# Performance work log

Measured on AMD Instinct MI355X. Metric: run time of the kernel, lower is better.

## Reference

```python
import jax, jax.numpy as jnp
import numpy as np

N = 100000      # nodes
E = 1600000     # edges (avg degree 16)
D_IN, HID, D_OUT = 128, 64, 64


def setup_inputs() -> dict:
    key = jax.random.key(0)
    ks = jax.random.split(key, 32)
    rn = lambda k, shape, s=0.1: jax.random.normal(k, shape, jnp.float32) * s
    inp = {
        "x": jax.random.normal(ks[0], (N, D_IN), jnp.float32),
        "edge_index": jax.random.randint(ks[1], (2, E), 0, N, dtype=jnp.int32),
        # GAT layer 1: in=128, heads=2, C=64, concat -> 128
        "w1": rn(ks[2], (D_IN, 2 * HID)), "as1": rn(ks[3], (2, HID)),
        "ad1": rn(ks[4], (2, HID)), "b1": rn(ks[5], (2 * HID,)),
        # GAT layer 2: in=128, heads=2, C=64, concat -> 128
        "w2": rn(ks[6], (2 * HID, 2 * HID)), "as2": rn(ks[7], (2, HID)),
        "ad2": rn(ks[8], (2, HID)), "b2": rn(ks[9], (2 * HID,)),
        # GAT layer 3: in=128, heads=1, C=64, mean -> 64
        "w3": rn(ks[10], (2 * HID, D_OUT)), "as3": rn(ks[11], (1, D_OUT)),
        "ad3": rn(ks[12], (1, D_OUT)), "b3": rn(ks[13], (D_OUT,)),
        # BatchNorm (eval mode: running stats)
        "g1": 1.0 + rn(ks[14], (2 * HID,)), "be1": rn(ks[15], (2 * HID,)),
        "m1": rn(ks[16], (2 * HID,), 0.01), "v1": 1.0 + 0.1 * jax.random.uniform(ks[17], (2 * HID,)),
        "g2": 1.0 + rn(ks[18], (2 * HID,)), "be2": rn(ks[19], (2 * HID,)),
        "m2": rn(ks[20], (2 * HID,), 0.01), "v2": 1.0 + 0.1 * jax.random.uniform(ks[21], (2 * HID,)),
        "g3": 1.0 + rn(ks[22], (D_OUT,)), "be3": rn(ks[23], (D_OUT,)),
        "m3": rn(ks[24], (D_OUT,), 0.01), "v3": 1.0 + 0.1 * jax.random.uniform(ks[25], (D_OUT,)),
    }
    return inp


def _gat(h, W, a_s, a_d, b, src, dst, n, heads, concat):
    """PyG GATConv (eval, add_self_loops already applied to src/dst)."""
    C = a_s.shape[1]
    xl = (h @ W).reshape(n, heads, C)                      # [N,H,C]
    es = jnp.sum(xl * a_s, axis=-1)                        # [N,H] att_src . x
    ed = jnp.sum(xl * a_d, axis=-1)                        # [N,H]
    e = jax.nn.leaky_relu(es[src] + ed[dst], 0.2)          # [E',H]
    mx = jax.ops.segment_max(e, dst, num_segments=n)       # segment softmax over dst
    ex = jnp.exp(e - mx[dst])
    den = jax.ops.segment_sum(ex, dst, num_segments=n)
    alpha = ex / (den[dst] + 1e-16)                        # [E',H]
    out = jax.ops.segment_sum(xl[src] * alpha[:, :, None], dst, num_segments=n)
    out = out.reshape(n, heads * C) if concat else out.mean(axis=1)
    return out + b


def _bn(z, g, be, m, v):
    return (z - m) * jax.lax.rsqrt(v + 1e-5) * g + be


def reference(x, edge_index, w1, as1, ad1, b1, w2, as2, ad2, b2, w3, as3, ad3, b3,
              g1, be1, m1, v1, g2, be2, m2, v2, g3, be3, m3, v3):
    n = x.shape[0]
    loop = jnp.arange(n, dtype=edge_index.dtype)
    src = jnp.concatenate([edge_index[0], loop])           # GATConv add_self_loops=True
    dst = jnp.concatenate([edge_index[1], loop])
    z = jax.nn.relu(_bn(_gat(x, w1, as1, ad1, b1, src, dst, n, 2, True), g1, be1, m1, v1))
    z = jax.nn.relu(_bn(_gat(z, w2, as2, ad2, b2, src, dst, n, 2, True), g2, be2, m2, v2))
    z = _bn(_gat(z, w3, as3, ad3, b3, src, dst, n, 1, False), g3, be3, m3, v3)
    return z
```

## Files before the change

kernel.cpp:

```cpp
#include <hip/hip_runtime.h>
#include <hip/hip_bf16.h>
#include <cstdint>
#include <cstddef>

#define SCAN_CHUNK 2048
#define NBLK 512
#define BSH 8

typedef short bf16x8 __attribute__((ext_vector_type(8)));
typedef float f32x4 __attribute__((ext_vector_type(4)));

__device__ __forceinline__ float leaky02(float x) { return x > 0.f ? x : 0.2f * x; }
__device__ __forceinline__ float bflo(unsigned u) { return __uint_as_float(u << 16); }
__device__ __forceinline__ float bfhi(unsigned u) { return __uint_as_float(u & 0xFFFF0000u); }
__device__ __forceinline__ unsigned short f2bf(float f) {
  __hip_bfloat16 h = __float2bfloat16(f);
  return *(unsigned short*)&h;
}
__device__ __forceinline__ unsigned pack2bf(float a, float b) {
  return (unsigned)f2bf(a) | ((unsigned)f2bf(b) << 16);
}

__global__ void scan_pass1(const int* __restrict__ cnt, int* __restrict__ bsum, int n) {
  __shared__ int red[4];
  int b = blockIdx.x, t = threadIdx.x;
  int base = b * SCAN_CHUNK;
  int s = 0;
  for (int i = t; i < SCAN_CHUNK; i += 256) {
    int idx = base + i;
    if (idx < n) s += cnt[idx];
  }
  for (int off = 32; off; off >>= 1) s += __shfl_xor(s, off);
  int lane = t & 63, wid = t >> 6;
  if (lane == 0) red[wid] = s;
  __syncthreads();
  if (t == 0) bsum[b] = red[0] + red[1] + red[2] + red[3];
}

__global__ void scan_pass2(int* __restrict__ bsum, int nb, int* __restrict__ totp) {
  if (threadIdx.x == 0) {
    int run = 0;
    for (int i = 0; i < nb; ++i) { int v = bsum[i]; bsum[i] = run; run += v; }
    *totp = run;
  }
}

__global__ void scan_pass3(const int* __restrict__ cnt, const int* __restrict__ bsum,
                           int* __restrict__ out, int n) {
  __shared__ int wsum[4];
  int b = blockIdx.x, t = threadIdx.x;
  int idx0 = b * SCAN_CHUNK + t * 8;
  int vals[8];
  int s = 0;
#pragma unroll
  for (int i = 0; i < 8; ++i) {
    int id = idx0 + i;
    int v = (id < n) ? cnt[id] : 0;
    vals[i] = s; s += v;
  }
  int lane = t & 63, wid = t >> 6;
  int incl = s;
  for (int off = 1; off < 64; off <<= 1) {
    int o = __shfl_up(incl, off);
    if (lane >= off) incl += o;
  }
  if (lane == 63) wsum[wid] = incl;
  __syncthreads();
  if (t == 0) { int r = 0; for (int i = 0; i < 4; ++i) { int v = wsum[i]; wsum[i] = r; r += v; } }
  __syncthreads();
  int texcl = incl - s + wsum[wid] + bsum[b];
#pragma unroll
  for (int i = 0; i < 8; ++i) {
    int id = idx0 + i;
    if (id < n) out[id] = texcl + vals[i];
  }
}

__global__ void bucketA(const int* __restrict__ dst, int* __restrict__ H,
                        int E, int N, int NB, int echunk, int nchunk) {
  __shared__ int hist[512];
  int b = blockIdx.x, t = threadIdx.x;
  hist[t] = 0; hist[t + 256] = 0;
  __syncthreads();
  int e0 = b * echunk, e1 = min(E, e0 + echunk);
  for (int e = e0 + t; e < e1; e += 256) atomicAdd(&hist[dst[e] >> BSH], 1);
  int n0 = b * nchunk, n1 = min(N, n0 + nchunk);
  for (int nn = n0 + t; nn < n1; nn += 256) atomicAdd(&hist[nn >> BSH], 1);
  __syncthreads();
  for (int k = t; k < NB; k += 256) H[k * NBLK + b] = hist[k];
}

__global__ void bucketB(const int* __restrict__ src, const int* __restrict__ dst,
                        const int* __restrict__ O, unsigned* __restrict__ binned,
                        int E, int N, int NB, int echunk, int nchunk) {
  __shared__ int cur[512];
  int b = blockIdx.x, t = threadIdx.x;
  for (int k = t; k < NB; k += 256) cur[k] = O[k * NBLK + b];
  __syncthreads();
  int e0 = b * echunk, e1 = min(E, e0 + echunk);
  for (int e = e0 + t; e < e1; e += 256) {
    int d = dst[e];
    int k = d >> BSH;
    int pos = atomicAdd(&cur[k], 1);
    binned[pos] = (unsigned)src[e] | ((unsigned)(d & 255) << 24);
  }
  int n0 = b * nchunk, n1 = min(N, n0 + nchunk);
  for (int nn = n0 + t; nn < n1; nn += 256) {
    int k = nn >> BSH;
    int pos = atomicAdd(&cur[k], 1);
    binned[pos] = (unsigned)nn | ((unsigned)(nn & 255) << 24);
  }
}

__global__ void bucketC(const unsigned* __restrict__ binned, const int* __restrict__ O,
                        int* __restrict__ rowp, int* __restrict__ col,
                        int N, int Etot, int NB) {
  __shared__ int cnt2[256];
  __shared__ int cur2[256];
  __shared__ int wsum[4];
  int k = blockIdx.x, t = threadIdx.x;
  int base = O[k * NBLK];
  int end  = (k + 1 < NB) ? O[(k + 1) * NBLK] : Etot;
  cnt2[t] = 0;
  __syncthreads();
  for (int e = base + t; e < end; e += 256) atomicAdd(&cnt2[binned[e] >> 24], 1);
  __syncthreads();
  int v = cnt2[t];
  int incl = v;
  int lane = t & 63, wid = t >> 6;
  for (int off = 1; off < 64; off <<= 1) {
    int o = __shfl_up(incl, off);
    if (lane >= off) incl += o;
  }
  if (lane == 63) wsum[wid] = incl;
  __syncthreads();
  if (t == 0) { int r = 0; for (int i = 0; i < 4; ++i) { int x2 = wsum[i]; wsum[i] = r; r += x2; } }
  __syncthreads();
  int excl = incl - v + wsum[wid];
  int g = (k << BSH) + t;
  if (g <= N) rowp[g] = base + excl;
  cur2[t] = excl;
  __syncthreads();
  for (int e = base + t; e < end; e += 256) {
    unsigned p = binned[e];
    int pos = atomicAdd(&cur2[p >> 24], 1);
    col[base + pos] = (int)(p & 0xFFFFFFu);
  }
}

__global__ void prep_w(const float* __restrict__ w1, const float* __restrict__ w2,
                       const float* __restrict__ w3,
                       unsigned short* __restrict__ t1, unsigned short* __restrict__ t2,
                       unsigned short* __restrict__ t3) {
  int b = blockIdx.x, t = threadIdx.x;
  const float* W; unsigned short* T; int NO; int e;
  if (b < 64)      { W = w1; T = t1; NO = 128; e = b * 256 + t; }
  else if (b < 128){ W = w2; T = t2; NO = 128; e = (b - 64) * 256 + t; }
  else             { W = w3; T = t3; NO = 64;  e = (b - 128) * 256 + t; }
  int c = e >> 7, k = e & 127;
  T[c * 128 + k] = f2bf(W[k * NO + c]);
}

template<int NO, bool F32IN>
__launch_bounds__(256)
__global__ void gemm_mfma(const void* __restrict__ Xp,
                          const unsigned short* __restrict__ Wt,
                          unsigned short* __restrict__ Y, int n,
                          const float* __restrict__ as, const float* __restrict__ ad,
                          float* __restrict__ es, float* __restrict__ ed) {
  constexpr int NT = NO / 16;
  const int wid = threadIdx.x >> 6, lane = threadIdx.x & 63;
  const int wr0 = (blockIdx.x * 4 + wid) * 32;
  if (wr0 >= n) return;
  const int cl = lane & 15, kg = lane >> 4;

  int r0c = wr0 + cl;      if (r0c > n - 1) r0c = n - 1;
  int r1c = wr0 + 16 + cl; if (r1c > n - 1) r1c = n - 1;

  f32x4 acc[2][NT] = {};
  const unsigned short* Xb = (const unsigned short*)Xp;
  const float* Xf = (const float*)Xp;

#pragma unroll
  for (int ks = 0; ks < 4; ++ks) {
    bf16x8 a0, a1;
    if constexpr (F32IN) {
      const float* p0 = Xf + (size_t)r0c * 128 + kg * 8 + ks * 32;
      const float* p1 = Xf + (size_t)r1c * 128 + kg * 8 + ks * 32;
      float4 u0 = *(const float4*)p0, u1 = *(const float4*)(p0 + 4);
      float4 w0 = *(const float4*)p1, w1 = *(const float4*)(p1 + 4);
      a0[0] = (short)f2bf(u0.x); a0[1] = (short)f2bf(u0.y); a0[2] = (short)f2bf(u0.z); a0[3] = (short)f2bf(u0.w);
      a0[4] = (short)f2bf(u1.x); a0[5] = (short)f2bf(u1.y); a0[6] = (short)f2bf(u1.z); a0[7] = (short)f2bf(u1.w);
      a1[0] = (short)f2bf(w0.x); a1[1] = (short)f2bf(w0.y); a1[2] = (short)f2bf(w0.z); a1[3] = (short)f2bf(w0.w);
// ... 18 lines not shown
  for (int s = 0; s < 2; ++s) {
#pragma unroll
    for (int rg = 0; rg < 4; ++rg) {
      int r = wr0 + s * 16 + kg * 4 + rg;
      float ps0 = 0.f, pd0 = 0.f, ps1 = 0.f, pd1 = 0.f;
#pragma unroll
      for (int t = 0; t < NT; ++t) {
        float a = acc[s][t][rg];
        if (NO == 128 && t >= 4) { ps1 = fmaf(a, asv[t], ps1); pd1 = fmaf(a, adv[t], pd1); }
        else                     { ps0 = fmaf(a, asv[t], ps0); pd0 = fmaf(a, adv[t], pd0); }
      }
#pragma unroll
      for (int o = 8; o; o >>= 1) {
        ps0 += __shfl_xor(ps0, o); pd0 += __shfl_xor(pd0, o);
        if (NO == 128) { ps1 += __shfl_xor(ps1, o); pd1 += __shfl_xor(pd1, o); }
      }
      if (r < n) {
        if (cl == 0) {
          if (NO == 128) {
            es[(size_t)r * 2] = ps0; es[(size_t)r * 2 + 1] = ps1;
            ed[(size_t)r * 2] = pd0; ed[(size_t)r * 2 + 1] = pd1;
          } else {
            es[r] = ps0; ed[r] = pd0;
          }
        }
#pragma unroll
        for (int t = 0; t < NT; ++t)
          Y[(size_t)r * NO + t * 16 + cl] = f2bf(acc[s][t][rg]);
      }
    }
  }
}

__launch_bounds__(256)
__global__ void aggregate2(const unsigned short* __restrict__ xl, const float* __restrict__ es,
                           const float* __restrict__ ed, const int* __restrict__ rowp,
                           const int* __restrict__ col, const float* __restrict__ bias,
                           const float* __restrict__ g, const float* __restrict__ be,
                           const float* __restrict__ m, const float* __restrict__ v,
                           uint4* __restrict__ out, int n) {
  int node = (blockIdx.x * blockDim.x + threadIdx.x) >> 6;
  int lane = threadIdx.x & 63;
  if (node >= n) return;
  const uint4* xr = (const uint4*)xl;
  int beg = rowp[node], end = rowp[node + 1];
  float2 edv = *(const float2*)&ed[(size_t)node * 2];
  const int q = lane >> 4, hl = lane & 15;

  float acc[8] = {0.f, 0.f, 0.f, 0.f, 0.f, 0.f, 0.f, 0.f};
  float dl0 = 0.f, dl1 = 0.f;

  for (int cb = beg; cb < end; cb += 64) {
    int idx = cb + lane;
    int s = 0; float w0 = 0.f, w1 = 0.f;
    if (idx < end) {
      s = col[idx];
      float2 e2 = *(const float2*)&es[(size_t)s * 2];
      w0 = __expf(leaky02(e2.x + edv.x));
      w1 = __expf(leaky02(e2.y + edv.y));
    }
    dl0 += w0; dl1 += w1;
    int cend = end - cb; if (cend > 64) cend = 64;
    int i = 0;
    for (; i + 8 <= cend; i += 8) {
      int j0 = i + q, j1 = i + 4 + q;
      int s0 = __shfl(s, j0), s1 = __shfl(s, j1);
      uint4 v0 = xr[(size_t)s0 * 16 + hl];
      uint4 v1 = xr[(size_t)s1 * 16 + hl];
      float w00 = __shfl(w0, j0), w01 = __shfl(w1, j0);
      float w10 = __shfl(w0, j1), w11 = __shfl(w1, j1);
      float W0 = (hl < 8) ? w00 : w01;
      float W1 = (hl < 8) ? w10 : w11;
      acc[0] = fmaf(W0, bflo(v0.x), acc[0]); acc[1] = fmaf(W0, bfhi(v0.x), acc[1]);
      acc[2] = fmaf(W0, bflo(v0.y), acc[2]); acc[3] = fmaf(W0, bfhi(v0.y), acc[3]);
      acc[4] = fmaf(W0, bflo(v0.z), acc[4]); acc[5] = fmaf(W0, bfhi(v0.z), acc[5]);
      acc[6] = fmaf(W0, bflo(v0.w), acc[6]); acc[7] = fmaf(W0, bfhi(v0.w), acc[7]);
      acc[0] = fmaf(W1, bflo(v1.x), acc[0]); acc[1] = fmaf(W1, bfhi(v1.x), acc[1]);
      acc[2] = fmaf(W1, bflo(v1.y), acc[2]); acc[3] = fmaf(W1, bfhi(v1.y), acc[3]);
      acc[4] = fmaf(W1, bflo(v1.z), acc[4]); acc[5] = fmaf(W1, bfhi(v1.z), acc[5]);
      acc[6] = fmaf(W1, bflo(v1.w), acc[6]); acc[7] = fmaf(W1, bfhi(v1.w), acc[7]);
    }
    for (; i < cend; i += 4) {
      int j = i + q;
      int s0 = __shfl(s, j);
      uint4 v0 = xr[(size_t)s0 * 16 + hl];
      float w00 = __shfl(w0, j), w01 = __shfl(w1, j);
      float W0 = (hl < 8) ? w00 : w01;
      acc[0] = fmaf(W0, bflo(v0.x), acc[0]); acc[1] = fmaf(W0, bfhi(v0.x), acc[1]);
      acc[2] = fmaf(W0, bflo(v0.y), acc[2]); acc[3] = fmaf(W0, bfhi(v0.y), acc[3]);
      acc[4] = fmaf(W0, bflo(v0.z), acc[4]); acc[5] = fmaf(W0, bfhi(v0.z), acc[5]);
      acc[6] = fmaf(W0, bflo(v0.w), acc[6]); acc[7] = fmaf(W0, bfhi(v0.w), acc[7]);
    }
  }

#pragma unroll
  for (int k2 = 0; k2 < 8; ++k2) {
    acc[k2] += __shfl_xor(acc[k2], 16);
    acc[k2] += __shfl_xor(acc[k2], 32);
  }
#pragma unroll
  for (int o = 32; o; o >>= 1) { dl0 += __shfl_xor(dl0, o); dl1 += __shfl_xor(dl1, o); }

  if (q == 0) {
    int c0 = hl * 8;
    float den = (hl < 8) ? dl0 : dl1;
    float inv = 1.f / (den + 1e-16f);
    float4 bi0 = *(const float4*)&bias[c0], bi1 = *(const float4*)&bias[c0 + 4];
    float4 mm0 = *(const float4*)&m[c0],    mm1 = *(const float4*)&m[c0 + 4];
    float4 vv0 = *(const float4*)&v[c0],    vv1 = *(const float4*)&v[c0 + 4];
    float4 gg0 = *(const float4*)&g[c0],    gg1 = *(const float4*)&g[c0 + 4];
    float4 bb0 = *(const float4*)&be[c0],   bb1 = *(const float4*)&be[c0 + 4];
    float r0 = (acc[0] * inv + bi0.x - mm0.x) * rsqrtf(vv0.x + 1e-5f) * gg0.x + bb0.x;
    float r1 = (acc[1] * inv + bi0.y - mm0.y) * rsqrtf(vv0.y + 1e-5f) * gg0.y + bb0.y;
    float r2 = (acc[2] * inv + bi0.z - mm0.z) * rsqrtf(vv0.z + 1e-5f) * gg0.z + bb0.z;
    float r3 = (acc[3] * inv + bi0.w - mm0.w) * rsqrtf(vv0.w + 1e-5f) * gg0.w + bb0.w;
    float r4 = (acc[4] * inv + bi1.x - mm1.x) * rsqrtf(vv1.x + 1e-5f) * gg1.x + bb1.x;
    float r5 = (acc[5] * inv + bi1.y - mm1.y) * rsqrtf(vv1.y + 1e-5f) * gg1.y + bb1.y;
    float r6 = (acc[6] * inv + bi1.z - mm1.z) * rsqrtf(vv1.z + 1e-5f) * gg1.z + bb1.z;
    float r7 = (acc[7] * inv + bi1.w - mm1.w) * rsqrtf(vv1.w + 1e-5f) * gg1.w + bb1.w;
    uint4 o;
    o.x = pack2bf(fmaxf(r0, 0.f), fmaxf(r1, 0.f));
    o.y = pack2bf(fmaxf(r2, 0.f), fmaxf(r3, 0.f));
    o.z = pack2bf(fmaxf(r4, 0.f), fmaxf(r5, 0.f));
    o.w = pack2bf(fmaxf(r6, 0.f), fmaxf(r7, 0.f));
    out[(size_t)node * 16 + hl] = o;
  }
}

__launch_bounds__(256)
__global__ void aggregate1(const unsigned short* __restrict__ xl, const float* __restrict__ es,
                           const float* __restrict__ ed, const int* __restrict__ rowp,
                           const int* __restrict__ col, const float* __restrict__ bias,
                           const float* __restrict__ g, const float* __restrict__ be,
                           const float* __restrict__ m, const float* __restrict__ v,
                           float* __restrict__ out, int n) {
  int node = (blockIdx.x * blockDim.x + threadIdx.x) >> 6;
  int lane = threadIdx.x & 63;
  if (node >= n) return;
  const uint4* xr = (const uint4*)xl;
  int beg = rowp[node], end = rowp[node + 1];
  float edv = ed[node];
  const int g8 = lane >> 3, hl = lane & 7;

  float acc[8] = {0.f, 0.f, 0.f, 0.f, 0.f, 0.f, 0.f, 0.f};
  float dl = 0.f;

  for (int cb = beg; cb < end; cb += 64) {
    int idx = cb + lane;
    int s = 0; float w = 0.f;
    if (idx < end) {
      s = col[idx];
      w = __expf(leaky02(es[s] + edv));
    }
    dl += w;
    int cend = end - cb; if (cend > 64) cend = 64;
    int i = 0;
    for (; i + 16 <= cend; i += 16) {
      int j0 = i + g8, j1 = i + 8 + g8;
// ... 59 lines not shown
  const float* x   = (const float*)d_in[0];
  const int*   ei  = (const int*)d_in[1];
  const float* w1  = (const float*)d_in[2];
  const float* as1 = (const float*)d_in[3];
  const float* ad1 = (const float*)d_in[4];
  const float* b1  = (const float*)d_in[5];
  const float* w2  = (const float*)d_in[6];
  const float* as2 = (const float*)d_in[7];
  const float* ad2 = (const float*)d_in[8];
  const float* b2  = (const float*)d_in[9];
  const float* w3  = (const float*)d_in[10];
  const float* as3 = (const float*)d_in[11];
  const float* ad3 = (const float*)d_in[12];
  const float* b3  = (const float*)d_in[13];
  const float* g1  = (const float*)d_in[14];
  const float* be1 = (const float*)d_in[15];
  const float* m1  = (const float*)d_in[16];
  const float* v1  = (const float*)d_in[17];
  const float* g2  = (const float*)d_in[18];
  const float* be2 = (const float*)d_in[19];
  const float* m2  = (const float*)d_in[20];
  const float* v2  = (const float*)d_in[21];
  const float* g3  = (const float*)d_in[22];
  const float* be3 = (const float*)d_in[23];
  const float* m3  = (const float*)d_in[24];
  const float* v3  = (const float*)d_in[25];

  const int N = in_sizes[0] / 128;
  const int E = in_sizes[1] / 2;
  const int Etot = E + N;
  const int* srcp = ei;
  const int* dstp = ei + E;
  const int NB = (N + 255) >> BSH;
  const int M  = NB * NBLK;
  const int echunk = (E + NBLK - 1) / NBLK;
  const int nchunk = (N + NBLK - 1) / NBLK;

  size_t off = 0;
  auto carve = [&](size_t bytes) {
    void* p = (char*)d_ws + off;
    off += (bytes + 255) & ~(size_t)255;
    return p;
  };
  unsigned short* Xb  = (unsigned short*)carve((size_t)N * 128 * 2);
  unsigned short* Yb  = (unsigned short*)carve((size_t)N * 128 * 2);
  float* esb  = (float*)carve((size_t)N * 2 * 4);
  float* edb  = (float*)carve((size_t)N * 2 * 4);
  int*   rowp = (int*)carve((size_t)(N + 1) * 4);
  int*   col  = (int*)carve((size_t)Etot * 4);
  int*   H    = (int*)carve((size_t)M * 4);
  int*   O    = (int*)carve((size_t)M * 4);
  unsigned* binned = (unsigned*)carve((size_t)Etot * 4);
  int*   bsum = (int*)carve(256 * 4);
  int*   tot  = (int*)carve(4);
  unsigned short* Wt1 = (unsigned short*)carve(128 * 128 * 2);
  unsigned short* Wt2 = (unsigned short*)carve(128 * 128 * 2);
  unsigned short* Wt3 = (unsigned short*)carve(128 * 64 * 2);
  (void)ws_size; (void)n_in; (void)out_size;

  const int nb2 = (M + SCAN_CHUNK - 1) / SCAN_CHUNK;

  bucketA<<<NBLK, 256, 0, stream>>>(dstp, H, E, N, NB, echunk, nchunk);
  scan_pass1<<<nb2, 256, 0, stream>>>(H, bsum, M);
  scan_pass2<<<1, 64, 0, stream>>>(bsum, nb2, tot);
  scan_pass3<<<nb2, 256, 0, stream>>>(H, bsum, O, M);
  bucketB<<<NBLK, 256, 0, stream>>>(srcp, dstp, O, binned, E, N, NB, echunk, nchunk);
  bucketC<<<NB, 256, 0, stream>>>(binned, O, rowp, col, N, Etot, NB);
  prep_w<<<160, 256, 0, stream>>>(w1, w2, w3, Wt1, Wt2, Wt3);

  const int gemm_grid = (N + 127) / 128;
  const int agg_grid = (N + 3) / 4;

  gemm_mfma<128, true><<<gemm_grid, 256, 0, stream>>>(x, Wt1, Yb, N, as1, ad1, esb, edb);
  aggregate2<<<agg_grid, 256, 0, stream>>>(Yb, esb, edb, rowp, col, b1, g1, be1, m1, v1,
                                           (uint4*)Xb, N);
  gemm_mfma<128, false><<<gemm_grid, 256, 0, stream>>>(Xb, Wt2, Yb, N, as2, ad2, esb, edb);
  aggregate2<<<agg_grid, 256, 0, stream>>>(Yb, esb, edb, rowp, col, b2, g2, be2, m2, v2,
                                           (uint4*)Xb, N);
  gemm_mfma<64, false><<<gemm_grid, 256, 0, stream>>>(Xb, Wt3, Yb, N, as3, ad3, esb, edb);
  aggregate1<<<agg_grid, 256, 0, stream>>>(Yb, esb, edb, rowp, col, b3, g3, be3, m3, v3,
                                           (float*)d_out, N);
}
```

Measured before the change: 344.5 us.

## Fuse aggregation with next-layer GEMM and simplify CSR bucketing pipeline

Aggregation for layers 1 and 2 is fused with the following layer's MFMA projection. Each block aggregates 64 nodes into a shared-memory bf16 tile, then multiplies it by the next weight matrix and writes the next layer's features and attention logits. This removes a global round-trip of the intermediate activations and two kernel launches. The CSR build replaces the per-block histogram matrix and three-pass scan with global atomic bucket counts, a single-block scan and atomic cursor claiming, and the weight transpose is folded into the histogram kernel. The trade-offs are half-wave-per-node aggregation with narrower edge chunks, plus a nondeterministic edge order within each bucket.

Result: slower. 363.7 us (+5.6%).

```diff
diff --git a/kernel.cpp b/kernel.cpp
--- a/kernel.cpp
+++ b/kernel.cpp
@@ -3,7 +3,6 @@
 #include <cstdint>
 #include <cstddef>
 
-#define SCAN_CHUNK 2048
 #define NBLK 512
 #define BSH 8
 
@@ -21,65 +20,24 @@
   return (unsigned)f2bf(a) | ((unsigned)f2bf(b) << 16);
 }
 
-__global__ void scan_pass1(const int* __restrict__ cnt, int* __restrict__ bsum, int n) {
-  __shared__ int red[4];
+__global__ void bucket_hist(const int* __restrict__ dst, int* __restrict__ T,
+                            int E, int N, int NB, int echunk, int nchunk,
+                            const float* __restrict__ w1, const float* __restrict__ w2,
+                            const float* __restrict__ w3,
+                            unsigned short* __restrict__ t1, unsigned short* __restrict__ t2,
+                            unsigned short* __restrict__ t3) {
   int b = blockIdx.x, t = threadIdx.x;
-  int base = b * SCAN_CHUNK;
-  int s = 0;
-  for (int i = t; i < SCAN_CHUNK; i += 256) {
-    int idx = base + i;
-    if (idx < n) s += cnt[idx];
-  }
-  for (int off = 32; off; off >>= 1) s += __shfl_xor(s, off);
-  int lane = t & 63, wid = t >> 6;
-  if (lane == 0) red[wid] = s;
-  __syncthreads();
-  if (t == 0) bsum[b] = red[0] + red[1] + red[2] + red[3];
-}
-
-__global__ void scan_pass2(int* __restrict__ bsum, int nb, int* __restrict__ totp) {
-  if (threadIdx.x == 0) {
-    int run = 0;
-    for (int i = 0; i < nb; ++i) { int v = bsum[i]; bsum[i] = run; run += v; }
-    *totp = run;
-  }
-}
-
-__global__ void scan_pass3(const int* __restrict__ cnt, const int* __restrict__ bsum,
-                           int* __restrict__ out, int n) {
-  __shared__ int wsum[4];
-  int b = blockIdx.x, t = threadIdx.x;
-  int idx0 = b * SCAN_CHUNK + t * 8;
-  int vals[8];
-  int s = 0;
-#pragma unroll
-  for (int i = 0; i < 8; ++i) {
-    int id = idx0 + i;
-    int v = (id < n) ? cnt[id] : 0;
-    vals[i] = s; s += v;
-  }
-  int lane = t & 63, wid = t >> 6;
-  int incl = s;
-  for (int off = 1; off < 64; off <<= 1) {
-    int o = __shfl_up(incl, off);
-    if (lane >= off) incl += o;
-  }
-  if (lane == 63) wsum[wid] = incl;
-  __syncthreads();
-  if (t == 0) { int r = 0; for (int i = 0; i < 4; ++i) { int v = wsum[i]; wsum[i] = r; r += v; } }
-  __syncthreads();
-  int texcl = incl - s + wsum[wid] + bsum[b];
-#pragma unroll
-  for (int i = 0; i < 8; ++i) {
-    int id = idx0 + i;
-    if (id < n) out[id] = texcl + vals[i];
-  }
-}
-
-__global__ void bucketA(const int* __restrict__ dst, int* __restrict__ H,
-                        int E, int N, int NB, int echunk, int nchunk) {
+  if (b >= NBLK) {
+    int bb = b - NBLK;
+    const float* W; unsigned short* Tw; int NO; int e;
+    if (bb < 64)      { W = w1; Tw = t1; NO = 128; e = bb * 256 + t; }
+    else if (bb < 128){ W = w2; Tw = t2; NO = 128; e = (bb - 64) * 256 + t; }
+    else              { W = w3; Tw = t3; NO = 64;  e = (bb - 128) * 256 + t; }
+    int c = e >> 7, k = e & 127;
+    Tw[c * 128 + k] = f2bf(W[k * NO + c]);
+    return;
+  }
   __shared__ int hist[512];
-  int b = blockIdx.x, t = threadIdx.x;
   hist[t] = 0; hist[t + 256] = 0;
   __syncthreads();
   int e0 = b * echunk, e1 = min(E, e0 + echunk);
@@ -87,24 +45,53 @@
   int n0 = b * nchunk, n1 = min(N, n0 + nchunk);
   for (int nn = n0 + t; nn < n1; nn += 256) atomicAdd(&hist[nn >> BSH], 1);
   __syncthreads();
-  for (int k = t; k < NB; k += 256) H[k * NBLK + b] = hist[k];
-}
-
-__global__ void bucketB(const int* __restrict__ src, const int* __restrict__ dst,
-                        const int* __restrict__ O, unsigned* __restrict__ binned,
-                        int E, int N, int NB, int echunk, int nchunk) {
+  for (int k = t; k < NB; k += 256) if (hist[k]) atomicAdd(&T[k], hist[k]);
+}
+
+__global__ void scan_small(const int* __restrict__ T, int* __restrict__ B,
+                           int* __restrict__ C, int NB) {
+  __shared__ int wsum[8];
+  int t = threadIdx.x;
+  int val = (t < NB) ? T[t] : 0;
+  int lane = t & 63, wid = t >> 6;
+  int incl = val;
+  for (int off = 1; off < 64; off <<= 1) {
+    int o = __shfl_up(incl, off);
+    if (lane >= off) incl += o;
+  }
+  if (lane == 63) wsum[wid] = incl;
+  __syncthreads();
+  if (t == 0) { int r = 0; for (int i = 0; i < 8; ++i) { int x = wsum[i]; wsum[i] = r; r += x; } }
+  __syncthreads();
+  int excl = incl - val + wsum[wid];
+  if (t <= NB) B[t] = excl;
+  if (t < NB) C[t] = excl;
+}
+
+__global__ void bucketB2(const int* __restrict__ src, const int* __restrict__ dst,
+                         int* __restrict__ C, unsigned* __restrict__ binned,
+                         int E, int N, int NB, int echunk, int nchunk) {
+  __shared__ int hist[512];
   __shared__ int cur[512];
   int b = blockIdx.x, t = threadIdx.x;
-  for (int k = t; k < NB; k += 256) cur[k] = O[k * NBLK + b];
+  hist[t] = 0; hist[t + 256] = 0;
   __syncthreads();
   int e0 = b * echunk, e1 = min(E, e0 + echunk);
+  for (int e = e0 + t; e < e1; e += 256) atomicAdd(&hist[dst[e] >> BSH], 1);
+  int n0 = b * nchunk, n1 = min(N, n0 + nchunk);
+  for (int nn = n0 + t; nn < n1; nn += 256) atomicAdd(&hist[nn >> BSH], 1);
+  __syncthreads();
+  for (int k = t; k < 512; k += 256) {
+    int c = hist[k];
+    cur[k] = c ? atomicAdd(&C[k], c) : 0;
+  }
+  __syncthreads();
   for (int e = e0 + t; e < e1; e += 256) {
     int d = dst[e];
     int k = d >> BSH;
     int pos = atomicAdd(&cur[k], 1);
     binned[pos] = (unsigned)src[e] | ((unsigned)(d & 255) << 24);
   }
-  int n0 = b * nchunk, n1 = min(N, n0 + nchunk);
   for (int nn = n0 + t; nn < n1; nn += 256) {
     int k = nn >> BSH;
     int pos = atomicAdd(&cur[k], 1);
@@ -112,15 +99,14 @@
   }
 }
 
-__global__ void bucketC(const unsigned* __restrict__ binned, const int* __restrict__ O,
-                        int* __restrict__ rowp, int* __restrict__ col,
-                        int N, int Etot, int NB) {
+__global__ void bucketC2(const unsigned* __restrict__ binned, const int* __restrict__ B,
+                         int* __restrict__ rowp, int* __restrict__ col, int N) {
   __shared__ int cnt2[256];
   __shared__ int cur2[256];
   __shared__ int wsum[4];
   int k = blockIdx.x, t = threadIdx.x;
-  int base = O[k * NBLK];
-  int end  = (k + 1 < NB) ? O[(k + 1) * NBLK] : Etot;
+  int base = B[k];
+  int end  = B[k + 1];
   cnt2[t] = 0;
   __syncthreads();
   for (int e = base + t; e < end; e += 256) atomicAdd(&cnt2[binned[e] >> 24], 1);
@@ -146,19 +132,6 @@
     int pos = atomicAdd(&cur2[p >> 24], 1);
     col[base + pos] = (int)(p & 0xFFFFFFu);
   }
-}
-
-__global__ void prep_w(const float* __restrict__ w1, const float* __restrict__ w2,
-                       const float* __restrict__ w3,
-                       unsigned short* __restrict__ t1, unsigned short* __restrict__ t2,
-                       unsigned short* __restrict__ t3) {
-  int b = blockIdx.x, t = threadIdx.x;
-  const float* W; unsigned short* T; int NO; int e;
-  if (b < 64)      { W = w1; T = t1; NO = 128; e = b * 256 + t; }
-  else if (b < 128){ W = w2; T = t2; NO = 128; e = (b - 64) * 256 + t; }
-  else             { W = w3; T = t3; NO = 64;  e = (b - 128) * 256 + t; }
-  int c = e >> 7, k = e & 127;
-  T[c * 128 + k] = f2bf(W[k * NO + c]);
 }
 
 template<int NO, bool F32IN>
@@ -243,98 +216,170 @@
   }
 }
 
+template<int NOUT>
 __launch_bounds__(256)
-__global__ void aggregate2(const unsigned short* __restrict__ xl, const float* __restrict__ es,
-                           const float* __restrict__ ed, const int* __restrict__ rowp,
-                           const int* __restrict__ col, const float* __restrict__ bias,
-                           const float* __restrict__ g, const float* __restrict__ be,
-                           const float* __restrict__ m, const float* __restrict__ v,
-                           uint4* __restrict__ out, int n) {
-  int node = (blockIdx.x * blockDim.x + threadIdx.x) >> 6;
-  int lane = threadIdx.x & 63;
-  if (node >= n) return;
+__global__ void agg_gemm(const unsigned short* __restrict__ xl,
+                         const float* __restrict__ es, const float* __restrict__ ed,
+                         const int* __restrict__ rowp, const int* __restrict__ col,
+                         const float* __restrict__ bias,
+                         const float* __restrict__ g, const float* __restrict__ be,
+                         const float* __restrict__ m, const float* __restrict__ v,
+                         const unsigned short* __restrict__ Wt,
+                         const float* __restrict__ as2, const float* __restrict__ ad2,
+                         unsigned short* __restrict__ Y,
+                         float* __restrict__ es2, float* __restrict__ ed2,
+                         int n) {
+  __shared__ unsigned short Z[64][136];
+  const int wid = threadIdx.x >> 6, lane = threadIdx.x & 63;
+  const int h = lane >> 5, hl = lane & 31;
+  const int rl = hl >> 4, hl3 = hl & 15;
   const uint4* xr = (const uint4*)xl;
-  int beg = rowp[node], end = rowp[node + 1];
-  float2 edv = *(const float2*)&ed[(size_t)node * 2];
-  const int q = lane >> 4, hl = lane & 15;
-
-  float acc[8] = {0.f, 0.f, 0.f, 0.f, 0.f, 0.f, 0.f, 0.f};
-  float dl0 = 0.f, dl1 = 0.f;
-
-  for (int cb = beg; cb < end; cb += 64) {
-    int idx = cb + lane;
-    int s = 0; float w0 = 0.f, w1 = 0.f;
-    if (idx < end) {
-      s = col[idx];
-      float2 e2 = *(const float2*)&es[(size_t)s * 2];
-      w0 = __expf(leaky02(e2.x + edv.x));
-      w1 = __expf(leaky02(e2.y + edv.y));
-    }
-    dl0 += w0; dl1 += w1;
-    int cend = end - cb; if (cend > 64) cend = 64;
-    int i = 0;
-    for (; i + 8 <= cend; i += 8) {
-      int j0 = i + q, j1 = i + 4 + q;
-      int s0 = __shfl(s, j0), s1 = __shfl(s, j1);
-      uint4 v0 = xr[(size_t)s0 * 16 + hl];
-      uint4 v1 = xr[(size_t)s1 * 16 + hl];
-      float w00 = __shfl(w0, j0), w01 = __shfl(w1, j0);
-      float w10 = __shfl(w0, j1), w11 = __shfl(w1, j1);
-      float W0 = (hl < 8) ? w00 : w01;
-      float W1 = (hl < 8) ? w10 : w11;
-      acc[0] = fmaf(W0, bflo(v0.x), acc[0]); acc[1] = fmaf(W0, bfhi(v0.x), acc[1]);
-      acc[2] = fmaf(W0, bflo(v0.y), acc[2]); acc[3] = fmaf(W0, bfhi(v0.y), acc[3]);
-      acc[4] = fmaf(W0, bflo(v0.z), acc[4]); acc[5] = fmaf(W0, bfhi(v0.z), acc[5]);
-      acc[6] = fmaf(W0, bflo(v0.w), acc[6]); acc[7] = fmaf(W0, bfhi(v0.w), acc[7]);
-      acc[0] = fmaf(W1, bflo(v1.x), acc[0]); acc[1] = fmaf(W1, bfhi(v1.x), acc[1]);
-      acc[2] = fmaf(W1, bflo(v1.y), acc[2]); acc[3] = fmaf(W1, bfhi(v1.y), acc[3]);
-      acc[4] = fmaf(W1, bflo(v1.z), acc[4]); acc[5] = fmaf(W1, bfhi(v1.z), acc[5]);
-      acc[6] = fmaf(W1, bflo(v1.w), acc[6]); acc[7] = fmaf(W1, bfhi(v1.w), acc[7]);
-    }
-    for (; i < cend; i += 4) {
-      int j = i + q;
-      int s0 = __shfl(s, j);
-      uint4 v0 = xr[(size_t)s0 * 16 + hl];
-      float w00 = __shfl(w0, j), w01 = __shfl(w1, j);
-      float W0 = (hl < 8) ? w00 : w01;
-      acc[0] = fmaf(W0, bflo(v0.x), acc[0]); acc[1] = fmaf(W0, bfhi(v0.x), acc[1]);
-      acc[2] = fmaf(W0, bflo(v0.y), acc[2]); acc[3] = fmaf(W0, bfhi(v0.y), acc[3]);
-      acc[4] = fmaf(W0, bflo(v0.z), acc[4]); acc[5] = fmaf(W0, bfhi(v0.z), acc[5]);
-      acc[6] = fmaf(W0, bflo(v0.w), acc[6]); acc[7] = fmaf(W0, bfhi(v0.w), acc[7]);
-    }
-  }
-
-#pragma unroll
-  for (int k2 = 0; k2 < 8; ++k2) {
-    acc[k2] += __shfl_xor(acc[k2], 16);
-    acc[k2] += __shfl_xor(acc[k2], 32);
-  }
-#pragma unroll
-  for (int o = 32; o; o >>= 1) { dl0 += __shfl_xor(dl0, o); dl1 += __shfl_xor(dl1, o); }
-
-  if (q == 0) {
-    int c0 = hl * 8;
-    float den = (hl < 8) ? dl0 : dl1;
-    float inv = 1.f / (den + 1e-16f);
-    float4 bi0 = *(const float4*)&bias[c0], bi1 = *(const float4*)&bias[c0 + 4];
-    float4 mm0 = *(const float4*)&m[c0],    mm1 = *(const float4*)&m[c0 + 4];
-    float4 vv0 = *(const float4*)&v[c0],    vv1 = *(const float4*)&v[c0 + 4];
-    float4 gg0 = *(const float4*)&g[c0],    gg1 = *(const float4*)&g[c0 + 4];
-    float4 bb0 = *(const float4*)&be[c0],   bb1 = *(const float4*)&be[c0 + 4];
-    float r0 = (acc[0] * inv + bi0.x - mm0.x) * rsqrtf(vv0.x + 1e-5f) * gg0.x + bb0.x;
-    float r1 = (acc[1] * inv + bi0.y - mm0.y) * rsqrtf(vv0.y + 1e-5f) * gg0.y + bb0.y;
-    float r2 = (acc[2] * inv + bi0.z - mm0.z) * rsqrtf(vv0.z + 1e-5f) * gg0.z + bb0.z;
-    float r3 = (acc[3] * inv + bi0.w - mm0.w) * rsqrtf(vv0.w + 1e-5f) * gg0.w + bb0.w;
-    float r4 = (acc[4] * inv + bi1.x - mm1.x) * rsqrtf(vv1.x + 1e-5f) * gg1.x + bb1.x;
-    float r5 = (acc[5] * inv + bi1.y - mm1.y) * rsqrtf(vv1.y + 1e-5f) * gg1.y + bb1.y;
-    float r6 = (acc[6] * inv + bi1.z - mm1.z) * rsqrtf(vv1.z + 1e-5f) * gg1.z + bb1.z;
-    float r7 = (acc[7] * inv + bi1.w - mm1.w) * rsqrtf(vv1.w + 1e-5f) * gg1.w + bb1.w;
-    uint4 o;
-    o.x = pack2bf(fmaxf(r0, 0.f), fmaxf(r1, 0.f));
-    o.y = pack2bf(fmaxf(r2, 0.f), fmaxf(r3, 0.f));
-    o.z = pack2bf(fmaxf(r4, 0.f), fmaxf(r5, 0.f));
-    o.w = pack2bf(fmaxf(r6, 0.f), fmaxf(r7, 0.f));
-    out[(size_t)node * 16 + hl] = o;
+  const int nb0 = blockIdx.x * 64;
+
+  for (int rnd = 0; rnd < 8; ++rnd) {
+    int nd = nb0 + wid * 16 + rnd * 2 + h;
+    bool valid = nd < n;
+    int ndc = valid ? nd : n - 1;
+    int beg = rowp[ndc], end = rowp[ndc + 1];
+    float2 edv = *(const float2*)&ed[(size_t)ndc * 2];
+    float acc[8] = {0.f, 0.f, 0.f, 0.f, 0.f, 0.f, 0.f, 0.f};
+    float dl0 = 0.f, dl1 = 0.f;
+
+    for (int cb = beg; cb < end; cb += 32) {
+      int idx = cb + hl;
+      int s = 0; float w0 = 0.f, w1 = 0.f;
+      if (idx < end) {
+        s = col[idx];
+        float2 e2 = *(const float2*)&es[(size_t)s * 2];
+        w0 = __expf(leaky02(e2.x + edv.x));
+        w1 = __expf(leaky02(e2.y + edv.y));
+      }
+      dl0 += w0; dl1 += w1;
+      int cend = end - cb; if (cend > 32) cend = 32;
+      int i = 0;
+      for (; i + 4 <= cend; i += 4) {
+        int j0 = h * 32 + i + rl, j1 = h * 32 + i + 2 + rl;
+        int s0 = __shfl(s, j0), s1 = __shfl(s, j1);
+        float w00 = __shfl(w0, j0), w01 = __shfl(w1, j0);
+        float w10 = __shfl(w0, j1), w11 = __shfl(w1, j1);
+        uint4 v0 = xr[(size_t)s0 * 16 + hl3];
+        uint4 v1 = xr[(size_t)s1 * 16 + hl3];
+        float W0 = (hl3 < 8) ? w00 : w01;
+        float W1 = (hl3 < 8) ? w10 : w11;
+        acc[0] = fmaf(W0, bflo(v0.x), acc[0]); acc[1] = fmaf(W0, bfhi(v0.x), acc[1]);
+        acc[2] = fmaf(W0, bflo(v0.y), acc[2]); acc[3] = fmaf(W0, bfhi(v0.y), acc[3]);
+        acc[4] = fmaf(W0, bflo(v0.z), acc[4]); acc[5] = fmaf(W0, bfhi(v0.z), acc[5]);
+        acc[6] = fmaf(W0, bflo(v0.w), acc[6]); acc[7] = fmaf(W0, bfhi(v0.w), acc[7]);
+        acc[0] = fmaf(W1, bflo(v1.x), acc[0]); acc[1] = fmaf(W1, bfhi(v1.x), acc[1]);
+        acc[2] = fmaf(W1, bflo(v1.y), acc[2]); acc[3] = fmaf(W1, bfhi(v1.y), acc[3]);
+        acc[4] = fmaf(W1, bflo(v1.z), acc[4]); acc[5] = fmaf(W1, bfhi(v1.z), acc[5]);
+        acc[6] = fmaf(W1, bflo(v1.w), acc[6]); acc[7] = fmaf(W1, bfhi(v1.w), acc[7]);
+      }
+      for (; i + 2 <= cend; i += 2) {
+        int j = h * 32 + i + rl;
+        int s0 = __shfl(s, j);
+        float w00 = __shfl(w0, j), w01 = __shfl(w1, j);
+        uint4 v0 = xr[(size_t)s0 * 16 + hl3];
+        float W0 = (hl3 < 8) ? w00 : w01;
+        acc[0] = fmaf(W0, bflo(v0.x), acc[0]); acc[1] = fmaf(W0, bfhi(v0.x), acc[1]);
+        acc[2] = fmaf(W0, bflo(v0.y), acc[2]); acc[3] = fmaf(W0, bfhi(v0.y), acc[3]);
+        acc[4] = fmaf(W0, bflo(v0.z), acc[4]); acc[5] = fmaf(W0, bfhi(v0.z), acc[5]);
+        acc[6] = fmaf(W0, bflo(v0.w), acc[6]); acc[7] = fmaf(W0, bfhi(v0.w), acc[7]);
+      }
+      if (i < cend) {
+        int j = h * 32 + i;
+        int s0 = __shfl(s, j);
+        float w00 = __shfl(w0, j), w01 = __shfl(w1, j);
+        uint4 v0 = xr[(size_t)s0 * 16 + hl3];
+        float W0 = (hl3 < 8) ? w00 : w01;
+        if (rl) W0 = 0.f;
+        acc[0] = fmaf(W0, bflo(v0.x), acc[0]); acc[1] = fmaf(W0, bfhi(v0.x), acc[1]);
+        acc[2] = fmaf(W0, bflo(v0.y), acc[2]); acc[3] = fmaf(W0, bfhi(v0.y), acc[3]);
+        acc[4] = fmaf(W0, bflo(v0.z), acc[4]); acc[5] = fmaf(W0, bfhi(v0.z), acc[5]);
+        acc[6] = fmaf(W0, bflo(v0.w), acc[6]); acc[7] = fmaf(W0, bfhi(v0.w), acc[7]);
+      }
+    }
+#pragma unroll
+    for (int k2 = 0; k2 < 8; ++k2) acc[k2] += __shfl_xor(acc[k2], 16);
+#pragma unroll
+    for (int o = 16; o; o >>= 1) { dl0 += __shfl_xor(dl0, o); dl1 += __shfl_xor(dl1, o); }
+
+    if (rl == 0) {
+      int c0 = hl3 * 8;
+      float den = (hl3 < 8) ? dl0 : dl1;
+      float inv = 1.f / (den + 1e-16f);
+      float4 bi0 = *(const float4*)&bias[c0], bi1 = *(const float4*)&bias[c0 + 4];
+      float4 mm0 = *(const float4*)&m[c0],    mm1 = *(const float4*)&m[c0 + 4];
+      float4 vv0 = *(const float4*)&v[c0],    vv1 = *(const float4*)&v[c0 + 4];
+      float4 gg0 = *(const float4*)&g[c0],    gg1 = *(const float4*)&g[c0 + 4];
+      float4 bb0 = *(const float4*)&be[c0],   bb1 = *(const float4*)&be[c0 + 4];
+      float r0 = (acc[0] * inv + bi0.x - mm0.x) * rsqrtf(vv0.x + 1e-5f) * gg0.x + bb0.x;
+      float r1 = (acc[1] * inv + bi0.y - mm0.y) * rsqrtf(vv0.y + 1e-5f) * gg0.y + bb0.y;
+      float r2 = (acc[2] * inv + bi0.z - mm0.z) * rsqrtf(vv0.z + 1e-5f) * gg0.z + bb0.z;
+      float r3 = (acc[3] * inv + bi0.w - mm0.w) * rsqrtf(vv0.w + 1e-5f) * gg0.w + bb0.w;
+      float r4 = (acc[4] * inv + bi1.x - mm1.x) * rsqrtf(vv1.x + 1e-5f) * gg1.x + bb1.x;
+      float r5 = (acc[5] * inv + bi1.y - mm1.y) * rsqrtf(vv1.y + 1e-5f) * gg1.y + bb1.y;
+      float r6 = (acc[6] * inv + bi1.z - mm1.z) * rsqrtf(vv1.z + 1e-5f) * gg1.z + bb1.z;
+      float r7 = (acc[7] * inv + bi1.w - mm1.w) * rsqrtf(vv1.w + 1e-5f) * gg1.w + bb1.w;
+      uint4 o;
+      if (valid) {
+        o.x = pack2bf(fmaxf(r0, 0.f), fmaxf(r1, 0.f));
+        o.y = pack2bf(fmaxf(r2, 0.f), fmaxf(r3, 0.f));
+        o.z = pack2bf(fmaxf(r4, 0.f), fmaxf(r5, 0.f));
+        o.w = pack2bf(fmaxf(r6, 0.f), fmaxf(r7, 0.f));
+      } else {
+        o.x = 0; o.y = 0; o.z = 0; o.w = 0;
+      }
+      *(uint4*)&Z[wid * 16 + rnd * 2 + h][c0] = o;
+    }
+  }
+  __syncthreads();
+
+  constexpr int NT = NOUT / 16;
+  const int cl = lane & 15, kg = lane >> 4;
+  f32x4 acc2[NT] = {};
+  const unsigned short* zrow = &Z[wid * 16 + cl][0];
+#pragma unroll
+  for (int ks = 0; ks < 4; ++ks) {
+    bf16x8 a = *(const bf16x8*)(zrow + kg * 8 + ks * 32);
+#pragma unroll
+    for (int t = 0; t < NT; ++t) {
+      bf16x8 bb = *(const bf16x8*)(Wt + (size_t)(cl + t * 16) * 128 + kg * 8 + ks * 32);
+      acc2[t] = __builtin_amdgcn_mfma_f32_16x16x32_bf16(a, bb, acc2[t], 0, 0, 0);
+    }
+  }
+  float asv[NT], adv[NT];
+#pragma unroll
+  for (int t = 0; t < NT; ++t) { asv[t] = as2[t * 16 + cl]; adv[t] = ad2[t * 16 + cl]; }
+
+#pragma unroll
+  for (int rg = 0; rg < 4; ++rg) {
+    int r = nb0 + wid * 16 + kg * 4 + rg;
+    float ps0 = 0.f, pd0 = 0.f, ps1 = 0.f, pd1 = 0.f;
+#pragma unroll
+    for (int t = 0; t < NT; ++t) {
+      float a = acc2[t][rg];
+      if (NOUT == 128 && t >= 4) { ps1 = fmaf(a, asv[t], ps1); pd1 = fmaf(a, adv[t], pd1); }
+      else                       { ps0 = fmaf(a, asv[t], ps0); pd0 = fmaf(a, adv[t], pd0); }
+    }
+#pragma unroll
+    for (int o = 8; o; o >>= 1) {
+      ps0 += __shfl_xor(ps0, o); pd0 += __shfl_xor(pd0, o);
+      if (NOUT == 128) { ps1 += __shfl_xor(ps1, o); pd1 += __shfl_xor(pd1, o); }
+    }
+    if (r < n) {
+      if (cl == 0) {
+        if (NOUT == 128) {
+          es2[(size_t)r * 2] = ps0; es2[(size_t)r * 2 + 1] = ps1;
+          ed2[(size_t)r * 2] = pd0; ed2[(size_t)r * 2 + 1] = pd1;
+        } else {
+          es2[r] = ps0; ed2[r] = pd0;
+        }
+      }
+#pragma unroll
+      for (int t = 0; t < NT; ++t)
+        Y[(size_t)r * NOUT + t * 16 + cl] = f2bf(acc2[t][rg]);
+    }
   }
 }
 
@@ -460,7 +505,6 @@
   const int* srcp = ei;
   const int* dstp = ei + E;
   const int NB = (N + 255) >> BSH;
-  const int M  = NB * NBLK;
   const int echunk = (E + NBLK - 1) / NBLK;
   const int nchunk = (N + NBLK - 1) / NBLK;
 
@@ -470,42 +514,43 @@
     off += (bytes + 255) & ~(size_t)255;
     return p;
   };
-  unsigned short* Xb  = (unsigned short*)carve((size_t)N * 128 * 2);
-  unsigned short* Yb  = (unsigned short*)carve((size_t)N * 128 * 2);
-  float* esb  = (float*)carve((size_t)N * 2 * 4);
-  float* edb  = (float*)carve((size_t)N * 2 * 4);
+  unsigned short* xl1 = (unsigned short*)carve((size_t)N * 128 * 2);
+  unsigned short* xl2 = (unsigned short*)carve((size_t)N * 128 * 2);
+  float* es1 = (float*)carve((size_t)N * 2 * 4);
+  float* ed1 = (float*)carve((size_t)N * 2 * 4);
+  float* es2 = (float*)carve((size_t)N * 2 * 4);
+  float* ed2 = (float*)carve((size_t)N * 2 * 4);
+  float* es3 = (float*)carve((size_t)N * 4);
+  float* ed3 = (float*)carve((size_t)N * 4);
   int*   rowp = (int*)carve((size_t)(N + 1) * 4);
   int*   col  = (int*)carve((size_t)Etot * 4);
-  int*   H    = (int*)carve((size_t)M * 4);
-  int*   O    = (int*)carve((size_t)M * 4);
-  unsigned* binned = (unsigned*)carve((size_t)Etot * 4);
-  int*   bsum = (int*)carve(256 * 4);
-  int*   tot  = (int*)carve(4);
+  size_t u = (size_t)N * 64 * 2; size_t ub = (size_t)Etot * 4;
+  unsigned short* xl3 = (unsigned short*)carve(u > ub ? u : ub);
+  unsigned* binned = (unsigned*)xl3;
+  int* T = (int*)carve(512 * 4);
+  int* B = (int*)carve(513 * 4);
+  int* C = (int*)carve(512 * 4);
   unsigned short* Wt1 = (unsigned short*)carve(128 * 128 * 2);
   unsigned short* Wt2 = (unsigned short*)carve(128 * 128 * 2);
   unsigned short* Wt3 = (unsigned short*)carve(128 * 64 * 2);
   (void)ws_size; (void)n_in; (void)out_size;
 
-  const int nb2 = (M + SCAN_CHUNK - 1) / SCAN_CHUNK;
-
-  bucketA<<<NBLK, 256, 0, stream>>>(dstp, H, E, N, NB, echunk, nchunk);
-  scan_pass1<<<nb2, 256, 0, stream>>>(H, bsum, M);
-  scan_pass2<<<1, 64, 0, stream>>>(bsum, nb2, tot);
-  scan_pass3<<<nb2, 256, 0, stream>>>(H, bsum, O, M);
-  bucketB<<<NBLK, 256, 0, stream>>>(srcp, dstp, O, binned, E, N, NB, echunk, nchunk);
-  bucketC<<<NB, 256, 0, stream>>>(binned, O, rowp, col, N, Etot, NB);
-  prep_w<<<160, 256, 0, stream>>>(w1, w2, w3, Wt1, Wt2, Wt3);
+  hipMemsetAsync(T, 0, NB * 4, stream);
+  bucket_hist<<<NBLK + 160, 256, 0, stream>>>(dstp, T, E, N, NB, echunk, nchunk,
+                                              w1, w2, w3, Wt1, Wt2, Wt3);
+  scan_small<<<1, 512, 0, stream>>>(T, B, C, NB);
+  bucketB2<<<NBLK, 256, 0, stream>>>(srcp, dstp, C, binned, E, N, NB, echunk, nchunk);
+  bucketC2<<<NB, 256, 0, stream>>>(binned, B, rowp, col, N);
 
   const int gemm_grid = (N + 127) / 128;
-  const int agg_grid = (N + 3) / 4;
-
-  gemm_mfma<128, true><<<gemm_grid, 256, 0, stream>>>(x, Wt1, Yb, N, as1, ad1, esb, edb);
-  aggregate2<<<agg_grid, 256, 0, stream>>>(Yb, esb, edb, rowp, col, b1, g1, be1, m1, v1,
-                                           (uint4*)Xb, N);
-  gemm_mfma<128, false><<<gemm_grid, 256, 0, stream>>>(Xb, Wt2, Yb, N, as2, ad2, esb, edb);
-  aggregate2<<<agg_grid, 256, 0, stream>>>(Yb, esb, edb, rowp, col, b2, g2, be2, m2, v2,
-                                           (uint4*)Xb, N);
-  gemm_mfma<64, false><<<gemm_grid, 256, 0, stream>>>(Xb, Wt3, Yb, N, as3, ad3, esb, edb);
-  aggregate1<<<agg_grid, 256, 0, stream>>>(Yb, esb, edb, rowp, col, b3, g3, be3, m3, v3,
+  const int fuse_grid = (N + 63) / 64;
+  const int agg_grid  = (N + 3) / 4;
+
+  gemm_mfma<128, true><<<gemm_grid, 256, 0, stream>>>(x, Wt1, xl1, N, as1, ad1, es1, ed1);
+  agg_gemm<128><<<fuse_grid, 256, 0, stream>>>(xl1, es1, ed1, rowp, col, b1, g1, be1, m1, v1,
+                                               Wt2, as2, ad2, xl2, es2, ed2, N);
+  agg_gemm<64><<<fuse_grid, 256, 0, stream>>>(xl2, es2, ed2, rowp, col, b2, g2, be2, m2, v2,
+                                              Wt3, as3, ad3, xl3, es3, ed3, N);
+  aggregate1<<<agg_grid, 256, 0, stream>>>(xl3, es3, ed3, rowp, col, b3, g3, be3, m3, v3,
                                            (float*)d_out, N);
 }
```

## Replace per-block bucket offset scan with global atomic bucket counters

Applied to the files above, without the earlier changes.

The three-pass scan over a per-block bucket histogram matrix is replaced by one global per-bucket count array, built with atomics, plus a single-block scan. The scatter pass recomputes its local histogram and reserves ranges through global atomicAdd. Weight transposition is folded into the histogram launch as extra blocks. Together these cut several kernel launches and the large H/O matrices, at the cost of a redundant histogram pass and non-deterministic ordering of edges within each bucket.

After: 348.3 us. About the same (+1.1%).

```diff
diff --git a/kernel.cpp b/kernel.cpp
--- a/kernel.cpp
+++ b/kernel.cpp
@@ -3,7 +3,6 @@
 #include <cstdint>
 #include <cstddef>
 
-#define SCAN_CHUNK 2048
 #define NBLK 512
 #define BSH 8
 
@@ -21,65 +20,24 @@
   return (unsigned)f2bf(a) | ((unsigned)f2bf(b) << 16);
 }
 
-__global__ void scan_pass1(const int* __restrict__ cnt, int* __restrict__ bsum, int n) {
-  __shared__ int red[4];
+__global__ void bucket_hist(const int* __restrict__ dst, int* __restrict__ T,
+                            int E, int N, int NB, int echunk, int nchunk,
+                            const float* __restrict__ w1, const float* __restrict__ w2,
+                            const float* __restrict__ w3,
+                            unsigned short* __restrict__ t1, unsigned short* __restrict__ t2,
+                            unsigned short* __restrict__ t3) {
   int b = blockIdx.x, t = threadIdx.x;
-  int base = b * SCAN_CHUNK;
-  int s = 0;
-  for (int i = t; i < SCAN_CHUNK; i += 256) {
-    int idx = base + i;
-    if (idx < n) s += cnt[idx];
-  }
-  for (int off = 32; off; off >>= 1) s += __shfl_xor(s, off);
-  int lane = t & 63, wid = t >> 6;
-  if (lane == 0) red[wid] = s;
-  __syncthreads();
-  if (t == 0) bsum[b] = red[0] + red[1] + red[2] + red[3];
-}
-
-__global__ void scan_pass2(int* __restrict__ bsum, int nb, int* __restrict__ totp) {
-  if (threadIdx.x == 0) {
-    int run = 0;
-    for (int i = 0; i < nb; ++i) { int v = bsum[i]; bsum[i] = run; run += v; }
-    *totp = run;
-  }
-}
-
-__global__ void scan_pass3(const int* __restrict__ cnt, const int* __restrict__ bsum,
-                           int* __restrict__ out, int n) {
-  __shared__ int wsum[4];
-  int b = blockIdx.x, t = threadIdx.x;
-  int idx0 = b * SCAN_CHUNK + t * 8;
-  int vals[8];
-  int s = 0;
-#pragma unroll
-  for (int i = 0; i < 8; ++i) {
-    int id = idx0 + i;
-    int v = (id < n) ? cnt[id] : 0;
-    vals[i] = s; s += v;
-  }
-  int lane = t & 63, wid = t >> 6;
-  int incl = s;
-  for (int off = 1; off < 64; off <<= 1) {
-    int o = __shfl_up(incl, off);
-    if (lane >= off) incl += o;
-  }
-  if (lane == 63) wsum[wid] = incl;
-  __syncthreads();
-  if (t == 0) { int r = 0; for (int i = 0; i < 4; ++i) { int v = wsum[i]; wsum[i] = r; r += v; } }
-  __syncthreads();
-  int texcl = incl - s + wsum[wid] + bsum[b];
-#pragma unroll
-  for (int i = 0; i < 8; ++i) {
-    int id = idx0 + i;
-    if (id < n) out[id] = texcl + vals[i];
-  }
-}
-
-__global__ void bucketA(const int* __restrict__ dst, int* __restrict__ H,
-                        int E, int N, int NB, int echunk, int nchunk) {
+  if (b >= NBLK) {
+    int bb = b - NBLK;
+    const float* W; unsigned short* Tw; int NO; int e;
+    if (bb < 64)      { W = w1; Tw = t1; NO = 128; e = bb * 256 + t; }
+    else if (bb < 128){ W = w2; Tw = t2; NO = 128; e = (bb - 64) * 256 + t; }
+    else              { W = w3; Tw = t3; NO = 64;  e = (bb - 128) * 256 + t; }
+    int c = e >> 7, k = e & 127;
+    Tw[c * 128 + k] = f2bf(W[k * NO + c]);
+    return;
+  }
   __shared__ int hist[512];
-  int b = blockIdx.x, t = threadIdx.x;
   hist[t] = 0; hist[t + 256] = 0;
   __syncthreads();
   int e0 = b * echunk, e1 = min(E, e0 + echunk);
@@ -87,24 +45,53 @@
   int n0 = b * nchunk, n1 = min(N, n0 + nchunk);
   for (int nn = n0 + t; nn < n1; nn += 256) atomicAdd(&hist[nn >> BSH], 1);
   __syncthreads();
-  for (int k = t; k < NB; k += 256) H[k * NBLK + b] = hist[k];
-}
-
-__global__ void bucketB(const int* __restrict__ src, const int* __restrict__ dst,
-                        const int* __restrict__ O, unsigned* __restrict__ binned,
-                        int E, int N, int NB, int echunk, int nchunk) {
+  for (int k = t; k < NB; k += 256) if (hist[k]) atomicAdd(&T[k], hist[k]);
+}
+
+__global__ void scan_small(const int* __restrict__ T, int* __restrict__ B,
+                           int* __restrict__ C, int NB) {
+  __shared__ int wsum[8];
+  int t = threadIdx.x;
+  int val = (t < NB) ? T[t] : 0;
+  int lane = t & 63, wid = t >> 6;
+  int incl = val;
+  for (int off = 1; off < 64; off <<= 1) {
+    int o = __shfl_up(incl, off);
+    if (lane >= off) incl += o;
+  }
+  if (lane == 63) wsum[wid] = incl;
+  __syncthreads();
+  if (t == 0) { int r = 0; for (int i = 0; i < 8; ++i) { int x = wsum[i]; wsum[i] = r; r += x; } }
+  __syncthreads();
+  int excl = incl - val + wsum[wid];
+  if (t <= NB) B[t] = excl;
+  if (t < NB) C[t] = excl;
+}
+
+__global__ void bucketB2(const int* __restrict__ src, const int* __restrict__ dst,
+                         int* __restrict__ C, unsigned* __restrict__ binned,
+                         int E, int N, int NB, int echunk, int nchunk) {
+  __shared__ int hist[512];
   __shared__ int cur[512];
   int b = blockIdx.x, t = threadIdx.x;
-  for (int k = t; k < NB; k += 256) cur[k] = O[k * NBLK + b];
+  hist[t] = 0; hist[t + 256] = 0;
   __syncthreads();
   int e0 = b * echunk, e1 = min(E, e0 + echunk);
+  for (int e = e0 + t; e < e1; e += 256) atomicAdd(&hist[dst[e] >> BSH], 1);
+  int n0 = b * nchunk, n1 = min(N, n0 + nchunk);
+  for (int nn = n0 + t; nn < n1; nn += 256) atomicAdd(&hist[nn >> BSH], 1);
+  __syncthreads();
+  for (int k = t; k < 512; k += 256) {
+    int c = hist[k];
+    cur[k] = c ? atomicAdd(&C[k], c) : 0;
+  }
+  __syncthreads();
   for (int e = e0 + t; e < e1; e += 256) {
     int d = dst[e];
     int k = d >> BSH;
     int pos = atomicAdd(&cur[k], 1);
     binned[pos] = (unsigned)src[e] | ((unsigned)(d & 255) << 24);
   }
-  int n0 = b * nchunk, n1 = min(N, n0 + nchunk);
   for (int nn = n0 + t; nn < n1; nn += 256) {
     int k = nn >> BSH;
     int pos = atomicAdd(&cur[k], 1);
@@ -112,15 +99,14 @@
   }
 }
 
-__global__ void bucketC(const unsigned* __restrict__ binned, const int* __restrict__ O,
-                        int* __restrict__ rowp, int* __restrict__ col,
-                        int N, int Etot, int NB) {
+__global__ void bucketC2(const unsigned* __restrict__ binned, const int* __restrict__ B,
+                         int* __restrict__ rowp, int* __restrict__ col, int N) {
   __shared__ int cnt2[256];
   __shared__ int cur2[256];
   __shared__ int wsum[4];
   int k = blockIdx.x, t = threadIdx.x;
-  int base = O[k * NBLK];
-  int end  = (k + 1 < NB) ? O[(k + 1) * NBLK] : Etot;
+  int base = B[k];
+  int end  = B[k + 1];
   cnt2[t] = 0;
   __syncthreads();
   for (int e = base + t; e < end; e += 256) atomicAdd(&cnt2[binned[e] >> 24], 1);
@@ -146,19 +132,6 @@
     int pos = atomicAdd(&cur2[p >> 24], 1);
     col[base + pos] = (int)(p & 0xFFFFFFu);
   }
-}
-
-__global__ void prep_w(const float* __restrict__ w1, const float* __restrict__ w2,
-                       const float* __restrict__ w3,
-                       unsigned short* __restrict__ t1, unsigned short* __restrict__ t2,
-                       unsigned short* __restrict__ t3) {
-  int b = blockIdx.x, t = threadIdx.x;
-  const float* W; unsigned short* T; int NO; int e;
-  if (b < 64)      { W = w1; T = t1; NO = 128; e = b * 256 + t; }
-  else if (b < 128){ W = w2; T = t2; NO = 128; e = (b - 64) * 256 + t; }
-  else             { W = w3; T = t3; NO = 64;  e = (b - 128) * 256 + t; }
-  int c = e >> 7, k = e & 127;
-  T[c * 128 + k] = f2bf(W[k * NO + c]);
 }
 
 template<int NO, bool F32IN>
@@ -460,7 +433,6 @@
   const int* srcp = ei;
   const int* dstp = ei + E;
   const int NB = (N + 255) >> BSH;
-  const int M  = NB * NBLK;
   const int echunk = (E + NBLK - 1) / NBLK;
   const int nchunk = (N + NBLK - 1) / NBLK;
 
@@ -476,28 +448,24 @@
   float* edb  = (float*)carve((size_t)N * 2 * 4);
   int*   rowp = (int*)carve((size_t)(N + 1) * 4);
   int*   col  = (int*)carve((size_t)Etot * 4);
-  int*   H    = (int*)carve((size_t)M * 4);
-  int*   O    = (int*)carve((size_t)M * 4);
   unsigned* binned = (unsigned*)carve((size_t)Etot * 4);
-  int*   bsum = (int*)carve(256 * 4);
-  int*   tot  = (int*)carve(4);
+  int* T = (int*)carve(512 * 4);
+  int* B = (int*)carve(513 * 4);
+  int* C = (int*)carve(512 * 4);
   unsigned short* Wt1 = (unsigned short*)carve(128 * 128 * 2);
   unsigned short* Wt2 = (unsigned short*)carve(128 * 128 * 2);
   unsigned short* Wt3 = (unsigned short*)carve(128 * 64 * 2);
   (void)ws_size; (void)n_in; (void)out_size;
 
-  const int nb2 = (M + SCAN_CHUNK - 1) / SCAN_CHUNK;
-
-  bucketA<<<NBLK, 256, 0, stream>>>(dstp, H, E, N, NB, echunk, nchunk);
-  scan_pass1<<<nb2, 256, 0, stream>>>(H, bsum, M);
-  scan_pass2<<<1, 64, 0, stream>>>(bsum, nb2, tot);
-  scan_pass3<<<nb2, 256, 0, stream>>>(H, bsum, O, M);
-  bucketB<<<NBLK, 256, 0, stream>>>(srcp, dstp, O, binned, E, N, NB, echunk, nchunk);
-  bucketC<<<NB, 256, 0, stream>>>(binned, O, rowp, col, N, Etot, NB);
-  prep_w<<<160, 256, 0, stream>>>(w1, w2, w3, Wt1, Wt2, Wt3);
+  hipMemsetAsync(T, 0, NB * 4, stream);
+  bucket_hist<<<NBLK + 160, 256, 0, stream>>>(dstp, T, E, N, NB, echunk, nchunk,
+                                              w1, w2, w3, Wt1, Wt2, Wt3);
+  scan_small<<<1, 512, 0, stream>>>(T, B, C, NB);
+  bucketB2<<<NBLK, 256, 0, stream>>>(srcp, dstp, C, binned, E, N, NB, echunk, nchunk);
+  bucketC2<<<NB, 256, 0, stream>>>(binned, B, rowp, col, N);
 
   const int gemm_grid = (N + 127) / 128;
-  const int agg_grid = (N + 3) / 4;
+  const int agg_grid  = (N + 3) / 4;
 
   gemm_mfma<128, true><<<gemm_grid, 256, 0, stream>>>(x, Wt1, Yb, N, as1, ad1, esb, edb);
   aggregate2<<<agg_grid, 256, 0, stream>>>(Yb, esb, edb, rowp, col, b1, g1, be1, m1, v1,
```
